# Optimization experiments

Measured on AMD Instinct MI355X. Metric: run time of the kernel, lower is better.

Reference implementation:

```python
import jax, jax.numpy as jnp
import numpy as np

BS, D, NC, N, C, K = 8192, 1024, 64, 100000, 1000, 50


def setup_inputs() -> dict:
    key = jax.random.key(0)
    k1, k2, k3, k4, k5 = jax.random.split(key, 5)
    return {
        "train_embedding": jax.random.normal(k1, (BS, D), dtype=jnp.float32),
        # concept initialized uniform in [-0.5, 0.5] as in init_concept
        "concept": jax.random.uniform(k2, (D, NC), dtype=jnp.float32, minval=-0.5, maxval=0.5),
        "bank": jax.random.normal(k3, (N, D), dtype=jnp.float32),
        "W_h": jax.random.normal(k4, (D, C), dtype=jnp.float32) * 0.02,
        "b_h": jax.random.normal(k5, (C,), dtype=jnp.float32) * 0.02,
        "topk": K,
    }


def reference(train_embedding, concept, bank, W_h, b_h, topk):
    # h_x: linear classifier head
    def h_x(z):
        return z @ W_h + b_h

    # projection onto concept subspace: C (C^T C)^{-1} C^T
    G = concept.T @ concept                      # [nc, nc]
    proj_matrix = concept @ jnp.linalg.inv(G) @ concept.T  # [D, D]
    proj = train_embedding @ proj_matrix.T       # (proj_matrix @ X^T)^T -> [bs, D]
    y_pred = h_x(proj)                           # [bs, C]
    orig_pred = h_x(train_embedding)             # [bs, C]

    # batched per-concept Euclidean distance to the whole bank: [nc, N]
    bank_sq = jnp.sum(bank * bank, axis=1)       # [N]
    con_sq = jnp.sum(concept * concept, axis=0)  # [nc]
    d2 = con_sq[:, None] - 2.0 * (concept.T @ bank.T) + bank_sq[None, :]
    dist = jnp.sqrt(jnp.maximum(d2, 0.0))
    # topk SMALLEST distances per concept
    _, idx = jax.lax.top_k(-dist, topk)          # idx: [nc, k]
    knn = bank[idx]                              # [nc, k, D] gather

    # L_sparse_1: mean over concepts of (c . mean_k knn)
    dots = jnp.einsum('dn,nkd->n', concept, knn) / topk  # [nc]
    L_sparse_1 = jnp.mean(dots)

    nc = concept.shape[1]
    eye = jnp.eye(nc, dtype=concept.dtype)
    L_sparse_2 = jnp.mean(G * (1.0 - eye))       # off-diagonal mean
    norm_metrics = jnp.mean(G * eye)             # diagonal mean

    return (orig_pred, y_pred, L_sparse_1, L_sparse_2, norm_metrics)
```

## Files before the change

### kernel.cpp

```cpp
#include <hip/hip_runtime.h>
#include <cstddef>

#define BSZ   8192
#define DIM   1024
#define NCON  64
#define NBANK 100000
#define NCLS  1000
#define TOPK  50
#define NCHUNK 32
#define CHUNK  3125
#define CHUNKP 3328

#define Y_OFF 8192000
#define S_OFF 16384000

typedef __attribute__((ext_vector_type(8))) short bf16x8;
typedef __attribute__((ext_vector_type(4))) float f32x4;

__device__ __forceinline__ short f2bf(float x) {
    unsigned u = __builtin_bit_cast(unsigned, x);
    unsigned r = (u + 0x7fffu + ((u >> 16) & 1u)) >> 16;
    return (short)r;
}

__device__ __forceinline__ bf16x8 pack8(f32x4 a, f32x4 b) {
    bf16x8 p;
    p[0] = f2bf(a[0]); p[1] = f2bf(a[1]); p[2] = f2bf(a[2]); p[3] = f2bf(a[3]);
    p[4] = f2bf(b[0]); p[5] = f2bf(b[1]); p[6] = f2bf(b[2]); p[7] = f2bf(b[3]);
    return p;
}

__device__ __forceinline__ void gload16(const short* g, short* l) {
    __builtin_amdgcn_global_load_lds(
        (__attribute__((address_space(1))) void*)g,
        (__attribute__((address_space(3))) void*)l,
        16, 0, 0);
}

__global__ void __launch_bounds__(256) prep_kernel(const float* __restrict__ cpt,
                                                   const float* __restrict__ Wh,
                                                   short* __restrict__ WhT,
                                                   short* __restrict__ cptT) {
    __shared__ short Ts[64][65];
    int b = blockIdx.x;
    int t = threadIdx.x;
    if (b < 256) {
        int k0 = (b & 15) * 64, n0 = (b >> 4) * 64;
        #pragma unroll
        for (int i = 0; i < 16; ++i) {
            int u = i * 256 + t;
            int kL = u >> 6, nL = u & 63;
            int n = n0 + nL;
            Ts[kL][nL] = (n < NCLS) ? f2bf(Wh[(size_t)(k0 + kL) * NCLS + n]) : (short)0;
        }
        __syncthreads();
        #pragma unroll
        for (int i = 0; i < 16; ++i) {
            int u = i * 256 + t;
            int nL = u >> 6, kL = u & 63;
            WhT[(size_t)(n0 + nL) * DIM + k0 + kL] = Ts[kL][nL];
        }
    } else {
        int q = b - 256;
        #pragma unroll
        for (int i = 0; i < 16; ++i) {
            int u = q * 4096 + i * 256 + t;
            int d = u >> 6, n = u & 63;
            cptT[n * DIM + d] = f2bf(cpt[u]);
        }
    }
}

__global__ void __launch_bounds__(256) mid_kernel(const float* __restrict__ bank,
                                                  const float* __restrict__ X,
                                                  const short* __restrict__ cptT,
                                                  const short* __restrict__ WhT,
                                                  short* __restrict__ Xbf,
                                                  short* __restrict__ XCbf,
                                                  float* __restrict__ key,
                                                  float* __restrict__ bank_sq,
                                                  short* __restrict__ MbfT,
                                                  float* __restrict__ G,
                                                  short* __restrict__ invGbf) {
    __shared__ float rowk[64];
    __shared__ float fk[64];
    int b = blockIdx.x;
    int t = threadIdx.x;
    int wid = t >> 6, l = t & 63, lr = l & 15, lg = l >> 4;
    if (b < 782) {
        int j0 = b * 128;
        int j_[2]; bool v_[2];
        const float* brow[2];
        #pragma unroll
        for (int ni = 0; ni < 2; ++ni) {
            j_[ni] = j0 + wid * 32 + ni * 16 + lr;
            v_[ni] = j_[ni] < NBANK;
            brow[ni] = bank + (size_t)j_[ni] * DIM + lg * 8;
        }
        f32x4 acc[4][2] = {};
        float sq[2] = {0.f, 0.f};
        for (int kk = 0; kk < DIM; kk += 32) {
            bf16x8 af[4];
            #pragma unroll
            for (int mi = 0; mi < 4; ++mi)
                af[mi] = *(const bf16x8*)(cptT + (mi * 16 + lr) * DIM + kk + lg * 8);
            #pragma unroll
            for (int ni = 0; ni < 2; ++ni) {
                f32x4 a = v_[ni] ? *(const f32x4*)(brow[ni] + kk)     : f32x4{0.f, 0.f, 0.f, 0.f};
                f32x4 c = v_[ni] ? *(const f32x4*)(brow[ni] + kk + 4) : f32x4{0.f, 0.f, 0.f, 0.f};
                sq[ni] += a[0]*a[0] + a[1]*a[1] + a[2]*a[2] + a[3]*a[3]
                        + c[0]*c[0] + c[1]*c[1] + c[2]*c[2] + c[3]*c[3];
                bf16x8 bfr = pack8(a, c);
                #pragma unroll
                for (int mi = 0; mi < 4; ++mi)
                    acc[mi][ni] = __builtin_amdgcn_mfma_f32_16x16x32_bf16(af[mi], bfr, acc[mi][ni], 0, 0, 0);
            }
        }
        #pragma unroll
        for (int ni = 0; ni < 2; ++ni) {
            float s = sq[ni];
            s += __shfl_xor(s, 16);
            s += __shfl_xor(s, 32);
            sq[ni] = s;
            if (v_[ni] && lg == 0) bank_sq[j_[ni]] = s;
        }
        #pragma unroll
        for (int mi = 0; mi < 4; ++mi)
            #pragma unroll
            for (int ni = 0; ni < 2; ++ni)
                if (v_[ni]) {
                    #pragma unroll
                    for (int r = 0; r < 4; ++r) {
                        int m = mi * 16 + lg * 4 + r;
                        key[(size_t)m * NBANK + j_[ni]] = sq[ni] - 2.f * acc[mi][ni][r];
                    }
                }
    } else if (b < 790) {
        int c0 = (b - 782) * 128;
        f32x4 acc[4][2] = {};
        for (int kk = 0; kk < DIM; kk += 32) {
            bf16x8 af[4], bfr[2];
            #pragma unroll
            for (int mi = 0; mi < 4; ++mi)
                af[mi] = *(const bf16x8*)(cptT + (mi * 16 + lr) * DIM + kk + lg * 8);
            #pragma unroll
            for (int ni = 0; ni < 2; ++ni)
                bfr[ni] = *(const bf16x8*)(WhT + (size_t)(c0 + wid * 32 + ni * 16 + lr) * DIM + kk + lg * 8);
            #pragma unroll
            for (int mi = 0; mi < 4; ++mi)
                #pragma unroll
                for (int ni = 0; ni < 2; ++ni)
                    acc[mi][ni] = __builtin_amdgcn_mfma_f32_16x16x32_bf16(af[mi], bfr[ni], acc[mi][ni], 0, 0, 0);
        }
        #pragma unroll
        for (int mi = 0; mi < 4; ++mi)
            #pragma unroll
            for (int ni = 0; ni < 2; ++ni)
                #pragma unroll
                for (int r = 0; r < 4; ++r) {
                    int m = mi * 16 + lg * 4 + r;
                    int c = c0 + wid * 32 + ni * 16 + lr;
                    MbfT[(size_t)c * NCON + m] = f2bf(acc[mi][ni][r]);
                }
    } else if (b == 790) {
        f32x4 acc[4] = {};
        for (int kk = 0; kk < DIM; kk += 32) {
            bf16x8 af[4], bfr;
            #pragma unroll
            for (int mi = 0; mi < 4; ++mi)
                af[mi] = *(const bf16x8*)(cptT + (mi * 16 + lr) * DIM + kk + lg * 8);
            bfr = *(const bf16x8*)(cptT + (wid * 16 + lr) * DIM + kk + lg * 8);
            #pragma unroll
            for (int mi = 0; mi < 4; ++mi)
                acc[mi] = __builtin_amdgcn_mfma_f32_16x16x32_bf16(af[mi], bfr, acc[mi], 0, 0, 0);
        }
        #pragma unroll
        for (int mi = 0; mi < 4; ++mi)
            #pragma unroll
            for (int r = 0; r < 4; ++r)
                G[(mi * 16 + lg * 4 + r) * 64 + wid * 16 + lr] = acc[mi][r];
        __syncthreads();
        float myA[16];
        #pragma unroll
        for (int s = 0; s < 16; ++s) myA[s] = G[(4 * s + wid) * 64 + l];
        #pragma unroll
        for (int k = 0; k < 64; ++k) {
            if (wid == (k & 3)) rowk[l] = myA[k >> 2];
            if (l == k) {
                #pragma unroll
                for (int s = 0; s < 16; ++s) fk[4 * s + wid] = myA[s];
            }
            __syncthreads();
            float ip = 1.f / rowk[k];
            float rv = rowk[l];
            #pragma unroll
            for (int s = 0; s < 16; ++s) {
                int i = 4 * s + wid;
                float fv = fk[i];
                float nv;
                if (i == k && l == k)      nv = ip;
                else if (i == k)           nv = rv * ip;
                else if (l == k)           nv = -fv * ip;
                else                       nv = myA[s] - fv * (rv * ip);
                myA[s] = nv;
            }
            __syncthreads();
        }
        #pragma unroll
        for (int s = 0; s < 16; ++s) invGbf[(4 * s + wid) * 64 + l] = f2bf(myA[s]);
    } else {
        int r0 = (b - 791) * 128;
        int r_[2];
        const float* xrow[2];
        #pragma unroll
        for (int ni = 0; ni < 2; ++ni) {
            r_[ni] = r0 + wid * 32 + ni * 16 + lr;
            xrow[ni] = X + (size_t)r_[ni] * DIM + lg * 8;
        }
        f32x4 acc[4][2] = {};
        for (int kk = 0; kk < DIM; kk += 32) {
            bf16x8 af[4];
            #pragma unroll
            for (int mi = 0; mi < 4; ++mi)
                af[mi] = *(const bf16x8*)(cptT + (mi * 16 + lr) * DIM + kk + lg * 8);
            #pragma unroll
            for (int ni = 0; ni < 2; ++ni) {
                f32x4 a = *(const f32x4*)(xrow[ni] + kk);
                f32x4 c = *(const f32x4*)(xrow[ni] + kk + 4);
                bf16x8 pk = pack8(a, c);
                *(bf16x8*)(Xbf + (size_t)r_[ni] * DIM + kk + lg * 8) = pk;
                #pragma unroll
                for (int mi = 0; mi < 4; ++mi)
                    acc[mi][ni] = __builtin_amdgcn_mfma_f32_16x16x32_bf16(af[mi], pk, acc[mi][ni], 0, 0, 0);
            }
        }
        #pragma unroll
        for (int mi = 0; mi < 4; ++mi)
            #pragma unroll
            for (int ni = 0; ni < 2; ++ni)
                #pragma unroll
                for (int r = 0; r < 4; ++r) {
                    int m = mi * 16 + lg * 4 + r;
                    XCbf[(size_t)r_[ni] * NCON + m] = f2bf(acc[mi][ni][r]);
                }
    }
}

__global__ void __launch_bounds__(256) topA_kernel(const float* __restrict__ key,
                                                   float* __restrict__ cand_v,
                                                   int* __restrict__ cand_j,
                                                   const short* __restrict__ invGbf,
                                                   const short* __restrict__ MbfT,
                                                   short* __restrict__ M2T) {
    __shared__ float vals[CHUNKP];
    __shared__ float wv[4];
    __shared__ int wj[4];
    int b = blockIdx.x;
    int t = threadIdx.x;
    if (b < 2048) {
        int n = b >> 5;
        int c = b & 31;
        int base = c * CHUNK;
        const float* row = key + (size_t)n * NBANK + base;
        float lv = __builtin_inff();
        int lj = 0x7fffffff;
        #pragma unroll 13
        for (int i = 0; i < 13; ++i) {
            int j = t + i * 256;
            float v = (j < CHUNK) ? row[j] : __builtin_inff();
            vals[j] = v;
            if (v < lv) { lv = v; lj = j; }
        }
        __syncthreads();
        float* cv = cand_v + (size_t)b * TOPK;
        int* cj = cand_j + (size_t)b * TOPK;
        for (int it = 0; it < TOPK; ++it) {
            float bv = lv; int bj = lj;
            #pragma unroll
            for (int o = 32; o > 0; o >>= 1) {
                float ov = __shfl_down(bv, o);
                int oj = __shfl_down(bj, o);
                if (ov < bv || (ov == bv && oj < bj)) { bv = ov; bj = oj; }
            }
            if ((t & 63) == 0) { wv[t >> 6] = bv; wj[t >> 6] = bj; }
            __syncthreads();
            float gv = wv[0]; int gj = wj[0];
            #pragma unroll
            for (int w2 = 1; w2 < 4; ++w2)
                if (wv[w2] < gv || (wv[w2] == gv && wj[w2] < gj)) { gv = wv[w2]; gj = wj[w2]; }
            if (t == 0) { cv[it] = gv; cj[it] = base + gj; }
            if (t == (gj & 255)) {
                vals[gj] = __builtin_inff();
                lv = __builtin_inff(); lj = 0x7fffffff;
                #pragma unroll 13
                for (int i = 0; i < 13; ++i) {
                    int j = t + i * 256;
                    float v = vals[j];
                    if (v < lv) { lv = v; lj = j; }
                }
            }
            __syncthreads();
        }
    } else {
        int c0 = (b - 2048) * 128;
        int wid = t >> 6, l = t & 63, lr = l & 15, lg = l >> 4;
        f32x4 acc[4][2] = {};
        #pragma unroll
        for (int ks = 0; ks < 2; ++ks) {
            bf16x8 af[4], bfr[2];
            #pragma unroll
            for (int mi = 0; mi < 4; ++mi)
                af[mi] = *(const bf16x8*)(invGbf + (mi * 16 + lr) * NCON + ks * 32 + lg * 8);
            #pragma unroll
            for (int ni = 0; ni < 2; ++ni)
                bfr[ni] = *(const bf16x8*)(MbfT + (size_t)(c0 + wid * 32 + ni * 16 + lr) * NCON + ks * 32 + lg * 8);
            #pragma unroll
            for (int mi = 0; mi < 4; ++mi)
                #pragma unroll
                for (int ni = 0; ni < 2; ++ni)
                    acc[mi][ni] = __builtin_amdgcn_mfma_f32_16x16x32_bf16(af[mi], bfr[ni], acc[mi][ni], 0, 0, 0);
        }
        #pragma unroll
        for (int mi = 0; mi < 4; ++mi)
            #pragma unroll
            for (int ni = 0; ni < 2; ++ni)
                #pragma unroll
                for (int r = 0; r < 4; ++r) {
                    int n = mi * 16 + lg * 4 + r;
                    int c = c0 + wid * 32 + ni * 16 + lr;
                    M2T[(size_t)c * NCON + n] = f2bf(acc[mi][ni][r]);
                }
    }
}

__global__ void __launch_bounds__(256) pred_kernel(const short* __restrict__ Xbf,
                                                   const short* __restrict__ WhT,
                                                   const short* __restrict__ XCbf,
                                                   const short* __restrict__ M2T,
                                                   const float* __restrict__ bh,
                                                   const float* __restrict__ cand_v,
                                                   const int* __restrict__ cand_j,
                                                   const float* __restrict__ bank_sq,
                                                   float* __restrict__ orig,
                                                   float* __restrict__ ypred,
                                                   float* __restrict__ dots) {
    __shared__ __align__(16) char smem[32768];
    int b = blockIdx.x;
    int t = threadIdx.x;
    int wid = t >> 6, l = t & 63, lr = l & 15, lg = l >> 4;
    if (b < 512) {
        short* As = (short*)smem;
        short* Bs = (short*)(smem + 16384);
        int c0 = (b & 7) * 128;
        int r0 = (b >> 3) * 128;
        int wr = wid >> 1, wc = wid & 1;
        int srow_off = l >> 3;
        int scol = ((l & 7) ^ (l >> 3)) * 8;
        f32x4 acc[4][4] = {};
        for (int kk = 0; kk < DIM; kk += 64) {
            if (kk) __syncthreads();
            #pragma unroll
            for (int i = 0; i < 4; ++i) {
                int si = wid * 4 + i;
                int row = si * 8 + srow_off;
                gload16(Xbf + (size_t)(r0 + row) * DIM + kk + scol, As + si * 512);
                gload16(WhT + (size_t)(c0 + row) * DIM + kk + scol, Bs + si * 512);
            }
            __syncthreads();
            #pragma unroll
            for (int ks = 0; ks < 2; ++ks) {
                bf16x8 af[4], bfr[4];
                #pragma unroll
                for (int mi = 0; mi < 4; ++mi) {
                    int rr = wr * 64 + mi * 16 + lr;
                    int slot = (ks * 4 + lg) ^ (rr & 7);
                    af[mi] = *(const bf16x8*)(As + rr * 64 + slot * 8);
                }
                #pragma unroll
                for (int ni = 0; ni < 4; ++ni) {
                    int cc = wc * 64 + ni * 16 + lr;
                    int slot = (ks * 4 + lg) ^ (cc & 7);
                    bfr[ni] = *(const bf16x8*)(Bs + cc * 64 + slot * 8);
                }
                #pragma unroll
                for (int mi = 0; mi < 4; ++mi)
                    #pragma unroll
                    for (int ni = 0; ni < 4; ++ni)
                        acc[mi][ni] = __builtin_amdgcn_mfma_f32_16x16x32_bf16(af[mi], bfr[ni], acc[mi][ni], 0, 0, 0);
            }
        }
        #pragma unroll
        for (int mi = 0; mi < 4; ++mi)
            #pragma unroll
            for (int ni = 0; ni < 4; ++ni) {
                int col = c0 + wc * 64 + ni * 16 + lr;
                if (col < NCLS) {
                    float bias = bh[col];
                    #pragma unroll
                    for (int r = 0; r < 4; ++r) {
                        int row = r0 + wr * 64 + mi * 16 + lg * 4 + r;
                        orig[(size_t)row * NCLS + col] = acc[mi][ni][r] + bias;
                    }
                }
            }
    } else if (b < 1024) {
        int q = b - 512;
        int c0 = (q & 7) * 128;
        int r0 = (q >> 3) * 128;
        int wr = wid >> 1, wc = wid & 1;
        f32x4 acc[4][4] = {};
        #pragma unroll
        for (int ks = 0; ks < 2; ++ks) {
            bf16x8 af[4], bfr[4];
            #pragma unroll
            for (int mi = 0; mi < 4; ++mi)
                af[mi] = *(const bf16x8*)(XCbf + (size_t)(r0 + wr * 64 + mi * 16 + lr) * NCON + ks * 32 + lg * 8);
            #pragma unroll
            for (int ni = 0; ni < 4; ++ni)
                bfr[ni] = *(const bf16x8*)(M2T + (size_t)(c0 + wc * 64 + ni * 16 + lr) * NCON + ks * 32 + lg * 8);
            #pragma unroll
            for (int mi = 0; mi < 4; ++mi)
                #pragma unroll
                for (int ni = 0; ni < 4; ++ni)
                    acc[mi][ni] = __builtin_amdgcn_mfma_f32_16x16x32_bf16(af[mi], bfr[ni], acc[mi][ni], 0, 0, 0);
        }
        #pragma unroll
        for (int mi = 0; mi < 4; ++mi)
            #pragma unroll
            for (int ni = 0; ni < 4; ++ni) {
                int col = c0 + wc * 64 + ni * 16 + lr;
                if (col < NCLS) {
                    float bias = bh[col];
                    #pragma unroll
                    for (int r = 0; r < 4; ++r) {
                        int row = r0 + wr * 64 + mi * 16 + lg * 4 + r;
                        ypred[(size_t)row * NCLS + col] = acc[mi][ni][r] + bias;
                    }
                }
            }
    } else {
        int n = b - 1024;
        const int NC2 = NCHUNK * TOPK;
        float* vals = (float*)smem;
        int* gidx = (int*)(smem + 6400);
        float* wv = (float*)(smem + 12800);
        int* wj = (int*)(smem + 12816);
        int* wl = (int*)(smem + 12832);
        for (int j = t; j < NC2; j += 256) {
            vals[j] = cand_v[(size_t)n * NC2 + j];
            gidx[j] = cand_j[(size_t)n * NC2 + j];
        }
        __syncthreads();
        float sum = 0.f;
        for (int it = 0; it < TOPK; ++it) {
            float bv = __builtin_inff();
            int bj = 0x7fffffff;
            int bl = -1;
            #pragma unroll 7
            for (int j = t; j < NC2; j += 256) {
                float v = vals[j];
                int gj = gidx[j];
                if (v < bv || (v == bv && gj < bj)) { bv = v; bj = gj; bl = j; }
            }
            #pragma unroll
            for (int o = 32; o > 0; o >>= 1) {
                float ov = __shfl_down(bv, o);
                int oj = __shfl_down(bj, o);
                int ol = __shfl_down(bl, o);
                if (ov < bv || (ov == bv && oj < bj)) { bv = ov; bj = oj; bl = ol; }
            }
            if ((t & 63) == 0) { wv[t >> 6] = bv; wj[t >> 6] = bj; wl[t >> 6] = bl; }
            __syncthreads();
            if (t == 0) {
                #pragma unroll
                for (int w2 = 1; w2 < 4; ++w2)
                    if (wv[w2] < bv || (wv[w2] == bv && wj[w2] < bj)) { bv = wv[w2]; bj = wj[w2]; bl = wl[w2]; }
                sum += 0.5f * (bank_sq[bj] - bv);
                vals[bl] = __builtin_inff();
            }
            __syncthreads();
        }
        if (t == 0) dots[n] = sum / (float)TOPK;
    }
}

__global__ void __launch_bounds__(256) fin_kernel(const float* __restrict__ G,
                                                  const float* __restrict__ dots,
                                                  float* __restrict__ out3) {
    __shared__ float r1[256], r2[256], r3[256];
    int t = threadIdx.x;
    float sd = 0.f, so = 0.f;
    for (int u = t; u < 4096; u += 256) {
        float g = G[u];
        if ((u >> 6) == (u & 63)) sd += g; else so += g;
    }
    float s1 = (t < NCON) ? dots[t] : 0.f;
    r1[t] = sd; r2[t] = so; r3[t] = s1;
    __syncthreads();
    for (int o = 128; o > 0; o >>= 1) {
        if (t < o) { r1[t] += r1[t + o]; r2[t] += r2[t + o]; r3[t] += r3[t + o]; }
        __syncthreads();
    }
    if (t == 0) {
        out3[0] = r3[0] / 64.f;
        out3[1] = r2[0] / 4096.f;
        out3[2] = r1[0] / 4096.f;
    }
}

extern "C" void kernel_launch(void* const* d_in, const int* in_sizes, int n_in,
                              void* d_out, int out_size, void* d_ws, size_t ws_size,
                              hipStream_t stream) {
    const float* X    = (const float*)d_in[0];
    const float* cpt  = (const float*)d_in[1];
    const float* bank = (const float*)d_in[2];
    const float* Wh   = (const float*)d_in[3];
    const float* bh   = (const float*)d_in[4];
    float* out = (float*)d_out;

    float* orig  = out;
    float* ypred = out + Y_OFF;
    float* out3  = out + S_OFF;

    char* w = (char*)d_ws;
    short* Xbf    = (short*)(w);
    short* WhT    = (short*)(w + 16777216);
    short* cptT   = (short*)(w + 18874368);
    short* XCbf   = (short*)(w + 19005440);
    short* M2T    = (short*)(w + 20054016);
    float* key    = (float*)(w + 20185088);
    float* bank_sq= (float*)(w + 45785088);
    float* G      = (float*)(w + 46185472);
    short* invGbf = (short*)(w + 46201856);
    short* MbfT   = (short*)(w + 46210048);
    float* cand_v = (float*)(w + 46341120);
    int*   cand_j = (int*)  (w + 46750720);
    float* dots   = (float*)(w + 47160320);

    prep_kernel<<<272, 256, 0, stream>>>(cpt, Wh, WhT, cptT);
    mid_kernel<<<855, 256, 0, stream>>>(bank, X, cptT, WhT, Xbf, XCbf, key, bank_sq, MbfT, G, invGbf);
    topA_kernel<<<2056, 256, 0, stream>>>(key, cand_v, cand_j, invGbf, MbfT, M2T);
    pred_kernel<<<1088, 256, 0, stream>>>(Xbf, WhT, XCbf, M2T, bh, cand_v, cand_j, bank_sq, orig, ypred, dots);
    fin_kernel<<<1, 256, 0, stream>>>(G, dots, out3);
}
```

Baseline: 462.3 us.

## Halve rows per bank-distance block and prefetch bank rows two steps ahead

The bank-distance section of mid_kernel now gives each wave 16 bank rows instead of 32, doubling the block count from 782 to 1563 so more blocks are in flight on the memory-bound bank read. The inner loop also register-prefetches the bank slices two k-steps ahead to hide global load latency behind the MFMAs. The trade-off is that each block reloads the concept fragments for half as much work, which doubles concept-fragment traffic per bank row. The dispatch offsets for the other block roles are shifted to match.

```diff
diff --git a/kernel.cpp b/kernel.cpp
--- a/kernel.cpp
+++ b/kernel.cpp
@@ -10,6 +10,7 @@
 #define NCHUNK 32
 #define CHUNK  3125
 #define CHUNKP 3328
+#define NDIST 1563
 
 #define Y_OFF 8192000
 #define S_OFF 16384000
@@ -87,56 +88,47 @@
     int b = blockIdx.x;
     int t = threadIdx.x;
     int wid = t >> 6, l = t & 63, lr = l & 15, lg = l >> 4;
-    if (b < 782) {
-        int j0 = b * 128;
-        int j_[2]; bool v_[2];
-        const float* brow[2];
-        #pragma unroll
-        for (int ni = 0; ni < 2; ++ni) {
-            j_[ni] = j0 + wid * 32 + ni * 16 + lr;
-            v_[ni] = j_[ni] < NBANK;
-            brow[ni] = bank + (size_t)j_[ni] * DIM + lg * 8;
-        }
-        f32x4 acc[4][2] = {};
-        float sq[2] = {0.f, 0.f};
+    if (b < NDIST) {
+        int j = b * 64 + wid * 16 + lr;
+        bool jv = j < NBANK;
+        const float* brow = bank + (size_t)j * DIM + lg * 8;
+        f32x4 acc[4] = {};
+        float sq = 0.f;
+        f32x4 va0, vb0, va1, vb1;
+        va0 = jv ? *(const f32x4*)(brow)      : f32x4{0.f, 0.f, 0.f, 0.f};
+        vb0 = jv ? *(const f32x4*)(brow + 4)  : f32x4{0.f, 0.f, 0.f, 0.f};
+        va1 = jv ? *(const f32x4*)(brow + 32) : f32x4{0.f, 0.f, 0.f, 0.f};
+        vb1 = jv ? *(const f32x4*)(brow + 36) : f32x4{0.f, 0.f, 0.f, 0.f};
         for (int kk = 0; kk < DIM; kk += 32) {
+            int kn = (kk + 64 < DIM) ? kk + 64 : kk;
+            f32x4 na = jv ? *(const f32x4*)(brow + kn)     : f32x4{0.f, 0.f, 0.f, 0.f};
+            f32x4 nb = jv ? *(const f32x4*)(brow + kn + 4) : f32x4{0.f, 0.f, 0.f, 0.f};
             bf16x8 af[4];
             #pragma unroll
             for (int mi = 0; mi < 4; ++mi)
                 af[mi] = *(const bf16x8*)(cptT + (mi * 16 + lr) * DIM + kk + lg * 8);
-            #pragma unroll
-            for (int ni = 0; ni < 2; ++ni) {
-                f32x4 a = v_[ni] ? *(const f32x4*)(brow[ni] + kk)     : f32x4{0.f, 0.f, 0.f, 0.f};
-                f32x4 c = v_[ni] ? *(const f32x4*)(brow[ni] + kk + 4) : f32x4{0.f, 0.f, 0.f, 0.f};
-                sq[ni] += a[0]*a[0] + a[1]*a[1] + a[2]*a[2] + a[3]*a[3]
-                        + c[0]*c[0] + c[1]*c[1] + c[2]*c[2] + c[3]*c[3];
-                bf16x8 bfr = pack8(a, c);
-                #pragma unroll
-                for (int mi = 0; mi < 4; ++mi)
-                    acc[mi][ni] = __builtin_amdgcn_mfma_f32_16x16x32_bf16(af[mi], bfr, acc[mi][ni], 0, 0, 0);
-            }
-        }
-        #pragma unroll
-        for (int ni = 0; ni < 2; ++ni) {
-            float s = sq[ni];
-            s += __shfl_xor(s, 16);
-            s += __shfl_xor(s, 32);
-            sq[ni] = s;
-            if (v_[ni] && lg == 0) bank_sq[j_[ni]] = s;
-        }
-        #pragma unroll
-        for (int mi = 0; mi < 4; ++mi)
-            #pragma unroll
-            for (int ni = 0; ni < 2; ++ni)
-                if (v_[ni]) {
-                    #pragma unroll
-                    for (int r = 0; r < 4; ++r) {
-                        int m = mi * 16 + lg * 4 + r;
-                        key[(size_t)m * NBANK + j_[ni]] = sq[ni] - 2.f * acc[mi][ni][r];
-                    }
-                }
-    } else if (b < 790) {
-        int c0 = (b - 782) * 128;
+            sq += va0[0]*va0[0] + va0[1]*va0[1] + va0[2]*va0[2] + va0[3]*va0[3]
+                + vb0[0]*vb0[0] + vb0[1]*vb0[1] + vb0[2]*vb0[2] + vb0[3]*vb0[3];
+            bf16x8 pk = pack8(va0, vb0);
+            #pragma unroll
+            for (int mi = 0; mi < 4; ++mi)
+                acc[mi] = __builtin_amdgcn_mfma_f32_16x16x32_bf16(af[mi], pk, acc[mi], 0, 0, 0);
+            va0 = va1; vb0 = vb1; va1 = na; vb1 = nb;
+        }
+        sq += __shfl_xor(sq, 16);
+        sq += __shfl_xor(sq, 32);
+        if (jv && lg == 0) bank_sq[j] = sq;
+        #pragma unroll
+        for (int mi = 0; mi < 4; ++mi)
+            if (jv) {
+                #pragma unroll
+                for (int r = 0; r < 4; ++r) {
+                    int m = mi * 16 + lg * 4 + r;
+                    key[(size_t)m * NBANK + j] = sq - 2.f * acc[mi][r];
+                }
+            }
+    } else if (b < NDIST + 8) {
+        int c0 = (b - NDIST) * 128;
         f32x4 acc[4][2] = {};
         for (int kk = 0; kk < DIM; kk += 32) {
             bf16x8 af[4], bfr[2];
@@ -162,7 +154,7 @@
                     int c = c0 + wid * 32 + ni * 16 + lr;
                     MbfT[(size_t)c * NCON + m] = f2bf(acc[mi][ni][r]);
                 }
-    } else if (b == 790) {
+    } else if (b == NDIST + 8) {
         f32x4 acc[4] = {};
         for (int kk = 0; kk < DIM; kk += 32) {
             bf16x8 af[4], bfr;
@@ -209,7 +201,7 @@
         #pragma unroll
         for (int s = 0; s < 16; ++s) invGbf[(4 * s + wid) * 64 + l] = f2bf(myA[s]);
     } else {
-        int r0 = (b - 791) * 128;
+        int r0 = (b - (NDIST + 9)) * 128;
         int r_[2];
         const float* xrow[2];
         #pragma unroll
@@ -538,7 +530,7 @@
     float* dots   = (float*)(w + 47160320);
 
     prep_kernel<<<272, 256, 0, stream>>>(cpt, Wh, WhT, cptT);
-    mid_kernel<<<855, 256, 0, stream>>>(bank, X, cptT, WhT, Xbf, XCbf, key, bank_sq, MbfT, G, invGbf);
+    mid_kernel<<<NDIST + 9 + 64, 256, 0, stream>>>(bank, X, cptT, WhT, Xbf, XCbf, key, bank_sq, MbfT, G, invGbf);
     topA_kernel<<<2056, 256, 0, stream>>>(key, cand_v, cand_j, invGbf, MbfT, M2T);
     pred_kernel<<<1088, 256, 0, stream>>>(Xbf, WhT, XCbf, M2T, bh, cand_v, cand_j, bank_sq, orig, ypred, dots);
     fin_kernel<<<1, 256, 0, stream>>>(G, dots, out3);
```

New measurement: 493.9 us. +6.8%, slower.

## Stage bank GEMM tiles through double-buffered swizzled LDS with async global loads

Applied to the files above, without the earlier changes.

The bank-distance GEMM in mid_kernel now loads bank rows and concept tiles into LDS with global_load_lds, double-buffered across the K loop and XOR-swizzled to avoid bank conflicts, instead of direct per-lane global loads. Block ordering is also changed so the small Wh, Gram/inverse and X projection blocks come first and the bank blocks run last. The aim is to overlap memory traffic with MFMA work and get better-coalesced loads on the memory-bound 400MB bank read. In exchange each block uses 40KB of LDS, which can reduce occupancy, and there is a barrier every iteration.

```diff
diff --git a/kernel.cpp b/kernel.cpp
--- a/kernel.cpp
+++ b/kernel.cpp
@@ -30,7 +30,7 @@
     return p;
 }
 
-__device__ __forceinline__ void gload16(const short* g, short* l) {
+__device__ __forceinline__ void gload16(const void* g, void* l) {
     __builtin_amdgcn_global_load_lds(
         (__attribute__((address_space(1))) void*)g,
         (__attribute__((address_space(3))) void*)l,
@@ -82,61 +82,12 @@
                                                   short* __restrict__ MbfT,
                                                   float* __restrict__ G,
                                                   short* __restrict__ invGbf) {
-    __shared__ float rowk[64];
-    __shared__ float fk[64];
+    __shared__ __align__(16) char smem[40960];
     int b = blockIdx.x;
     int t = threadIdx.x;
     int wid = t >> 6, l = t & 63, lr = l & 15, lg = l >> 4;
-    if (b < 782) {
-        int j0 = b * 128;
-        int j_[2]; bool v_[2];
-        const float* brow[2];
-        #pragma unroll
-        for (int ni = 0; ni < 2; ++ni) {
-            j_[ni] = j0 + wid * 32 + ni * 16 + lr;
-            v_[ni] = j_[ni] < NBANK;
-            brow[ni] = bank + (size_t)j_[ni] * DIM + lg * 8;
-        }
-        f32x4 acc[4][2] = {};
-        float sq[2] = {0.f, 0.f};
-        for (int kk = 0; kk < DIM; kk += 32) {
-            bf16x8 af[4];
-            #pragma unroll
-            for (int mi = 0; mi < 4; ++mi)
-                af[mi] = *(const bf16x8*)(cptT + (mi * 16 + lr) * DIM + kk + lg * 8);
-            #pragma unroll
-            for (int ni = 0; ni < 2; ++ni) {
-                f32x4 a = v_[ni] ? *(const f32x4*)(brow[ni] + kk)     : f32x4{0.f, 0.f, 0.f, 0.f};
-                f32x4 c = v_[ni] ? *(const f32x4*)(brow[ni] + kk + 4) : f32x4{0.f, 0.f, 0.f, 0.f};
-                sq[ni] += a[0]*a[0] + a[1]*a[1] + a[2]*a[2] + a[3]*a[3]
-                        + c[0]*c[0] + c[1]*c[1] + c[2]*c[2] + c[3]*c[3];
-                bf16x8 bfr = pack8(a, c);
-                #pragma unroll
-                for (int mi = 0; mi < 4; ++mi)
-                    acc[mi][ni] = __builtin_amdgcn_mfma_f32_16x16x32_bf16(af[mi], bfr, acc[mi][ni], 0, 0, 0);
-            }
-        }
-        #pragma unroll
-        for (int ni = 0; ni < 2; ++ni) {
-            float s = sq[ni];
-            s += __shfl_xor(s, 16);
-            s += __shfl_xor(s, 32);
-            sq[ni] = s;
-            if (v_[ni] && lg == 0) bank_sq[j_[ni]] = s;
-        }
-        #pragma unroll
-        for (int mi = 0; mi < 4; ++mi)
-            #pragma unroll
-            for (int ni = 0; ni < 2; ++ni)
-                if (v_[ni]) {
-                    #pragma unroll
-                    for (int r = 0; r < 4; ++r) {
-                        int m = mi * 16 + lg * 4 + r;
-                        key[(size_t)m * NBANK + j_[ni]] = sq[ni] - 2.f * acc[mi][ni][r];
-                    }
-                }
-    } else if (b < 790) {
-        int c0 = (b - 782) * 128;
+    if (b < 8) {
+        int c0 = b * 128;
         f32x4 acc[4][2] = {};
         for (int kk = 0; kk < DIM; kk += 32) {
             bf16x8 af[4], bfr[2];
@@ -162,7 +113,9 @@
                     int c = c0 + wid * 32 + ni * 16 + lr;
                     MbfT[(size_t)c * NCON + m] = f2bf(acc[mi][ni][r]);
                 }
-    } else if (b == 790) {
+    } else if (b == 8) {
+        float* rowk = (float*)smem;
+        float* fk = (float*)(smem + 256);
         f32x4 acc[4] = {};
         for (int kk = 0; kk < DIM; kk += 32) {
             bf16x8 af[4], bfr;
@@ -208,8 +161,8 @@
         }
         #pragma unroll
         for (int s = 0; s < 16; ++s) invGbf[(4 * s + wid) * 64 + l] = f2bf(myA[s]);
-    } else {
-        int r0 = (b - 791) * 128;
+    } else if (b < 73) {
+        int r0 = (b - 9) * 128;
         int r_[2];
         const float* xrow[2];
         #pragma unroll
@@ -243,6 +196,88 @@
                     int m = mi * 16 + lg * 4 + r;
                     XCbf[(size_t)r_[ni] * NCON + m] = f2bf(acc[mi][ni][r]);
                 }
+    } else {
+        int j0 = (b - 73) * 128;
+        int bj[4], bs[4];
+        #pragma unroll
+        for (int i = 0; i < 4; ++i) {
+            int flat = i * 4096 + wid * 1024 + l * 16;
+            bj[i] = flat >> 7;
+            bs[i] = ((flat >> 4) & 7) ^ (bj[i] & 7);
+        }
+        int cflat = wid * 1024 + l * 16;
+        int cm = cflat >> 6;
+        int cs = ((cflat >> 4) & 3) ^ (cm & 3);
+        f32x4 acc[4][2] = {};
+        float sq[2] = {0.f, 0.f};
+        int jrow[2];
+        #pragma unroll
+        for (int ni = 0; ni < 2; ++ni) jrow[ni] = wid * 32 + ni * 16 + lr;
+        #pragma unroll
+        for (int i = 0; i < 4; ++i) {
+            int jr = j0 + bj[i]; if (jr >= NBANK) jr = NBANK - 1;
+            gload16(bank + (size_t)jr * DIM + bs[i] * 4, smem + i * 4096 + wid * 1024);
+        }
+        gload16(cptT + cm * DIM + cs * 8, smem + 32768 + wid * 1024);
+        int buf = 0;
+        for (int kk = 0; kk < DIM; kk += 32) {
+            __syncthreads();
+            int kn = kk + 32;
+            int nb = buf ^ 1;
+            if (kn < DIM) {
+                #pragma unroll
+                for (int i = 0; i < 4; ++i) {
+                    int jr = j0 + bj[i]; if (jr >= NBANK) jr = NBANK - 1;
+                    gload16(bank + (size_t)jr * DIM + kn + bs[i] * 4,
+                            smem + nb * 16384 + i * 4096 + wid * 1024);
+                }
+                gload16(cptT + cm * DIM + kn + cs * 8, smem + 32768 + nb * 4096 + wid * 1024);
+            }
+            const float* bT = (const float*)(smem + buf * 16384);
+            const short* cS = (const short*)(smem + 32768 + buf * 4096);
+            bf16x8 af[4];
+            #pragma unroll
+            for (int mi = 0; mi < 4; ++mi) {
+                int m = mi * 16 + lr;
+                af[mi] = *(const bf16x8*)(cS + m * 32 + ((lg ^ (m & 3)) << 3));
+            }
+            #pragma unroll
+            for (int ni = 0; ni < 2; ++ni) {
+                int j = jrow[ni];
+                int g0 = lg * 2, g1 = lg * 2 + 1;
+                f32x4 a = *(const f32x4*)(bT + j * 32 + ((g0 ^ (j & 7)) << 2));
+                f32x4 c = *(const f32x4*)(bT + j * 32 + ((g1 ^ (j & 7)) << 2));
+                sq[ni] += a[0]*a[0] + a[1]*a[1] + a[2]*a[2] + a[3]*a[3]
+                        + c[0]*c[0] + c[1]*c[1] + c[2]*c[2] + c[3]*c[3];
+                bf16x8 pk = pack8(a, c);
+                #pragma unroll
+                for (int mi = 0; mi < 4; ++mi)
+                    acc[mi][ni] = __builtin_amdgcn_mfma_f32_16x16x32_bf16(af[mi], pk, acc[mi][ni], 0, 0, 0);
+            }
+            buf ^= 1;
+        }
+        #pragma unroll
+        for (int ni = 0; ni < 2; ++ni) {
+            float s = sq[ni];
+            s += __shfl_xor(s, 16);
+            s += __shfl_xor(s, 32);
+            sq[ni] = s;
+            int j = j0 + jrow[ni];
+            if (j < NBANK && lg == 0) bank_sq[j] = s;
+        }
+        #pragma unroll
+        for (int mi = 0; mi < 4; ++mi)
+            #pragma unroll
+            for (int ni = 0; ni < 2; ++ni) {
+                int j = j0 + jrow[ni];
+                if (j < NBANK) {
+                    #pragma unroll
+                    for (int r = 0; r < 4; ++r) {
+                        int m = mi * 16 + lg * 4 + r;
+                        key[(size_t)m * NBANK + j] = sq[ni] - 2.f * acc[mi][ni][r];
+                    }
+                }
+            }
     }
 }
 
@@ -538,7 +573,7 @@
     float* dots   = (float*)(w + 47160320);
 
     prep_kernel<<<272, 256, 0, stream>>>(cpt, Wh, WhT, cptT);
-    mid_kernel<<<855, 256, 0, stream>>>(bank, X, cptT, WhT, Xbf, XCbf, key, bank_sq, MbfT, G, invGbf);
+    mid_kernel<<<73 + 782, 256, 0, stream>>>(bank, X, cptT, WhT, Xbf, XCbf, key, bank_sq, MbfT, G, invGbf);
     topA_kernel<<<2056, 256, 0, stream>>>(key, cand_v, cand_j, invGbf, MbfT, M2T);
     pred_kernel<<<1088, 256, 0, stream>>>(Xbf, WhT, XCbf, M2T, bh, cand_v, cand_j, bank_sq, orig, ypred, dots);
     fin_kernel<<<1, 256, 0, stream>>>(G, dots, out3);
```

Result: faster. 404.2 us (-12.6%).
